# Kernel tuning notes

Measured on AMD Instinct MI355X. Metric: run time of the kernel, lower is better.

The kernel has to match this reference:

```python
import jax, jax.numpy as jnp
import numpy as np

EPS = 1e-6
NUM_HEADS = 16

def _phi(x):
    # elu kernel feature map: elu(x) + 1 (ensures positivity)
    return jax.nn.elu(x) + 1.0

def setup_inputs() -> dict:
    key = jax.random.key(0)
    ks = jax.random.split(key, 5)
    B, S, D = 2, 2048, 1024
    scale = 1.0 / np.sqrt(D)  # mimic xavier-ish magnitude
    return {
        "x": jax.random.normal(ks[0], (B, S, D), dtype=jnp.float32),
        "Wq": jax.random.normal(ks[1], (D, D), dtype=jnp.float32) * scale,
        "bq": jnp.zeros((D,), dtype=jnp.float32),
        "Wk": jax.random.normal(ks[2], (D, D), dtype=jnp.float32) * scale,
        "bk": jnp.zeros((D,), dtype=jnp.float32),
        "Wv": jax.random.normal(ks[3], (D, D), dtype=jnp.float32) * scale,
        "bv": jnp.zeros((D,), dtype=jnp.float32),
        "Wo": jax.random.normal(ks[4], (D, D), dtype=jnp.float32) * scale,
        "bo": jnp.zeros((D,), dtype=jnp.float32),
    }

def reference(x, Wq, bq, Wk, bk, Wv, bv, Wo, bo):
    B, S, D = x.shape
    H = NUM_HEADS
    hd = D // H
    # projections (torch Linear: x @ W.T + b)
    q = (x @ Wq.T + bq).reshape(B, S, H, hd).transpose(0, 2, 1, 3)  # [B,H,S,d]
    k = (x @ Wk.T + bk).reshape(B, S, H, hd).transpose(0, 2, 1, 3)
    v = (x @ Wv.T + bv).reshape(B, S, H, hd).transpose(0, 2, 1, 3)
    q = _phi(q)
    k = _phi(k)
    # prefix sums of outer products k_t v_t^T and of k_t (causal linear attention)
    kv_cum = jnp.cumsum(k[..., :, None] * v[..., None, :], axis=2)  # [B,H,S,d,d]
    k_cum = jnp.cumsum(k, axis=2)                                   # [B,H,S,d]
    num = jnp.einsum('bhsd,bhsde->bhse', q, kv_cum)                 # [B,H,S,d]
    den = jnp.einsum('bhsd,bhsd->bhs', q, k_cum)                    # [B,H,S]
    out = num / (den[..., None] + EPS)
    out = out.transpose(0, 2, 1, 3).reshape(B, S, D)
    return out @ Wo.T + bo
```

## Files before the change

kernel.cpp:

```cpp
#include <hip/hip_runtime.h>

typedef unsigned short u16;
typedef __attribute__((ext_vector_type(8))) short bf16x8;
typedef __attribute__((ext_vector_type(4))) float f32x4;

#define DEVI static __device__ __forceinline__

DEVI u16 f2bf(float f) {
  union { float f; unsigned int u; } a; a.f = f;
  unsigned int u = a.u;
  u += 0x7fffu + ((u >> 16) & 1u);
  return (u16)(u >> 16);
}
DEVI float bf2f(u16 h) {
  union { unsigned int u; float f; } a; a.u = ((unsigned int)h) << 16;
  return a.f;
}

DEVI void gload_lds16(const u16* g, u16* l) {
  __builtin_amdgcn_global_load_lds(
      (const __attribute__((address_space(1))) void*)g,
      (__attribute__((address_space(3))) void*)l, 16, 0, 0);
}

DEVI int ldsIdx(int row, int col) {
  return ((col >> 5) << 11) + (row << 5) + (col & 31);
}

struct alignas(8) US4 { u16 a, b, c, d; };

__global__ __launch_bounds__(256) void k_cvt_all(
    const float* __restrict__ x, const float* __restrict__ Wq,
    const float* __restrict__ Wk, const float* __restrict__ Wv,
    const float* __restrict__ Wo, u16* __restrict__ xb, u16* __restrict__ Wqb,
    u16* __restrict__ Wkb, u16* __restrict__ Wvb, u16* __restrict__ Wob) {
  int i = blockIdx.x * 256 + threadIdx.x;
  const float* s;
  u16* d;
  int off;
  if (i < 1048576) {
    s = x; d = xb; off = i;
  } else {
    int j = i - 1048576;
    int w = j >> 18;
    off = j & 262143;
    s = (w == 0) ? Wq : (w == 1) ? Wk : (w == 2) ? Wv : Wo;
    d = (w == 0) ? Wqb : (w == 1) ? Wkb : (w == 2) ? Wvb : Wob;
  }
  f32x4 v = ((const f32x4*)s)[off];
  US4 o{f2bf(v[0]), f2bf(v[1]), f2bf(v[2]), f2bf(v[3])};
  ((US4*)d)[off] = o;
}

__global__ __launch_bounds__(256) void k_gemm_qkv(
    const u16* __restrict__ A, const u16* __restrict__ W,
    const float* __restrict__ bq, const float* __restrict__ bk,
    const float* __restrict__ bv, u16* __restrict__ qb, u16* __restrict__ kb,
    u16* __restrict__ ktb, u16* __restrict__ vtb) {
  __shared__ __align__(16) u16 As[128 * 32];
  __shared__ __align__(16) u16 Bs[128 * 32];
  const int tid = threadIdx.x;
  const int lane = tid & 63;
  const int wave = tid >> 6;
  const int wm = wave >> 1, wn = wave & 1;
  const int m0 = blockIdx.x * 128, n0 = blockIdx.y * 128;
  const int K = 1024;
  const int m = lane & 15, quad = lane >> 4;

  f32x4 acc[4][4];
#pragma unroll
  for (int i = 0; i < 4; i++)
#pragma unroll
    for (int j = 0; j < 4; j++) acc[i][j] = (f32x4){0.f, 0.f, 0.f, 0.f};

  const int r0 = tid >> 2;
  const int r1 = (tid + 256) >> 2;
  const int c0 = (((tid & 3) ^ (r0 & 3))) * 8;
  const u16* Ab0 = A + (size_t)(m0 + r0) * K + c0;
  const u16* Ab1 = A + (size_t)(m0 + r1) * K + c0;
  const u16* Bb0 = W + (size_t)(n0 + r0) * K + c0;
  const u16* Bb1 = W + (size_t)(n0 + r1) * K + c0;
  u16* lA0 = &As[tid * 8];
  u16* lA1 = &As[(tid + 256) * 8];
  u16* lB0 = &Bs[tid * 8];
  u16* lB1 = &Bs[(tid + 256) * 8];

  const int koff = (quad ^ (m & 3)) * 8;
  for (int k0 = 0; k0 < K; k0 += 32) {
    __syncthreads();
    gload_lds16(Ab0 + k0, lA0);
    gload_lds16(Ab1 + k0, lA1);
    gload_lds16(Bb0 + k0, lB0);
    gload_lds16(Bb1 + k0, lB1);
    __syncthreads();
    bf16x8 af[4], bfr[4];
#pragma unroll
    for (int t = 0; t < 4; t++) {
      af[t] = *(const bf16x8*)&As[(wm * 64 + t * 16 + m) * 32 + koff];
      bfr[t] = *(const bf16x8*)&Bs[(wn * 64 + t * 16 + m) * 32 + koff];
    }
#pragma unroll
    for (int i = 0; i < 4; i++)
#pragma unroll
      for (int j = 0; j < 4; j++)
        acc[i][j] = __builtin_amdgcn_mfma_f32_16x16x32_bf16(af[i], bfr[j],
                                                            acc[i][j], 0, 0, 0);
  }

  const int lr = quad * 4, lc = m;
  const int region = (int)(blockIdx.y >> 3);
  const float* bias = region == 0 ? bq : (region == 1 ? bk : bv);
#pragma unroll
  for (int j = 0; j < 4; j++) {
    const int colg = n0 + wn * 64 + j * 16 + lc;
    const int cl = colg - (region << 10);
    const float bvv = bias[cl];
#pragma unroll
    for (int i = 0; i < 4; i++) {
      const int row0 = m0 + wm * 64 + i * 16 + lr;
      float v4[4];
#pragma unroll
      for (int r = 0; r < 4; r++) {
        float v = acc[i][j][r] + bvv;
        if (region < 2) v = (v > 0.f) ? (v + 1.f) : __expf(v);
        v4[r] = v;
      }
      if (region == 0) {
#pragma unroll
        for (int r = 0; r < 4; r++)
          qb[(size_t)(row0 + r) * 1024 + cl] = f2bf(v4[r]);
      } else if (region == 1) {
#pragma unroll
        for (int r = 0; r < 4; r++)
          kb[(size_t)(row0 + r) * 1024 + cl] = f2bf(v4[r]);
        US4 o{f2bf(v4[0]), f2bf(v4[1]), f2bf(v4[2]), f2bf(v4[3])};
        *(US4*)&ktb[(size_t)cl * 4096 + row0] = o;
      } else {
        US4 o{f2bf(v4[0]), f2bf(v4[1]), f2bf(v4[2]), f2bf(v4[3])};
        *(US4*)&vtb[(size_t)cl * 4096 + row0] = o;
      }
    }
  }
}

__global__ __launch_bounds__(256) void k_gemm_out(const u16* __restrict__ A,
                                                  const u16* __restrict__ B,
                                                  const float* __restrict__ bias,
                                                  float* __restrict__ C) {
  __shared__ __align__(16) u16 As[64 * 32];
  __shared__ __align__(16) u16 Bs[128 * 32];
  const int tid = threadIdx.x;
  const int lane = tid & 63;
  const int wave = tid >> 6;
  const int wm = wave >> 1, wn = wave & 1;
  const int m0 = blockIdx.x * 64, n0 = blockIdx.y * 128;
  const int K = 1024, N = 1024;
  const int m = lane & 15, quad = lane >> 4;

  f32x4 acc[2][4];
#pragma unroll
  for (int i = 0; i < 2; i++)
#pragma unroll
    for (int j = 0; j < 4; j++) acc[i][j] = (f32x4){0.f, 0.f, 0.f, 0.f};

  const int ra = tid >> 2;
  const int rb1 = (tid + 256) >> 2;
  const int c0 = (((tid & 3) ^ (ra & 3))) * 8;
  const u16* Ap = A + (size_t)(m0 + ra) * K + c0;
  const u16* Bp0 = B + (size_t)(n0 + ra) * K + c0;
  const u16* Bp1 = B + (size_t)(n0 + rb1) * K + c0;
  u16* lA = &As[tid * 8];
  u16* lB0 = &Bs[tid * 8];
  u16* lB1 = &Bs[(tid + 256) * 8];

  const int koff = (quad ^ (m & 3)) * 8;
  for (int k0 = 0; k0 < K; k0 += 32) {
    __syncthreads();
    gload_lds16(Ap + k0, lA);
    gload_lds16(Bp0 + k0, lB0);
    gload_lds16(Bp1 + k0, lB1);
    __syncthreads();
    bf16x8 af[2], bfr[4];
#pragma unroll
    for (int i = 0; i < 2; i++)
      af[i] = *(const bf16x8*)&As[(wm * 32 + i * 16 + m) * 32 + koff];
#pragma unroll
    for (int j = 0; j < 4; j++)
      bfr[j] = *(const bf16x8*)&Bs[(wn * 64 + j * 16 + m) * 32 + koff];
#pragma unroll
    for (int i = 0; i < 2; i++)
#pragma unroll
      for (int j = 0; j < 4; j++)
        acc[i][j] = __builtin_amdgcn_mfma_f32_16x16x32_bf16(af[i], bfr[j],
                                                            acc[i][j], 0, 0, 0);
  }

#pragma unroll
  for (int j = 0; j < 4; j++) {
    const int col = n0 + wn * 64 + j * 16 + m;
    const float bv = bias[col];
#pragma unroll
    for (int i = 0; i < 2; i++) {
      const int row = m0 + wm * 32 + i * 16 + quad * 4;
#pragma unroll
      for (int r = 0; r < 4; r++)
        C[(size_t)(row + r) * N + col] = acc[i][j][r] + bv;
    }
  }
}

__global__ __launch_bounds__(256) void k_chunk2(const u16* __restrict__ ktb,
                                                const u16* __restrict__ vtb,
                                                u16* __restrict__ KVtb,
                                                float* __restrict__ Ks) {
  __shared__ __align__(16) u16 Kt[4096];
  __shared__ __align__(16) u16 Vt[4096];
  __shared__ __align__(16) u16 Ct[64 * 72];
  __shared__ float ksp[64][4];
  const int tid = threadIdx.x, lane = tid & 63, wave = tid >> 6;
  const int ci = blockIdx.x, h = blockIdx.y, b = blockIdx.z;
  const int t0 = b * 2048 + ci * 64, dB = h * 64;
  const int c = (b * 16 + h) * 32 + ci;
  const int row = tid >> 2, colr = (tid & 3) * 8;
#pragma unroll
  for (int r = 0; r < 2; r++) {
    const int col = r * 32 + colr;
    gload_lds16(ktb + (size_t)(dB + row) * 4096 + t0 + col, Kt + r * 2048 + tid * 8);
    gload_lds16(vtb + (size_t)(dB + row) * 4096 + t0 + col, Vt + r * 2048 + tid * 8);
  }
  __syncthreads();
  {
    const int rr = tid >> 2, part = tid & 3;
    float s = 0.f;
#pragma unroll
    for (int t = 0; t < 16; t++) s += bf2f(Kt[ldsIdx(rr, part * 16 + t)]);
    ksp[rr][part] = s;
  }
  __syncthreads();
  if (tid < 64)
    Ks[c * 64 + tid] = ksp[tid][0] + ksp[tid][1] + ksp[tid][2] + ksp[tid][3];

  const int wm = wave >> 1, wn = wave & 1;
  const int md0 = wm * 32, ne0 = wn * 32;
  const int m = lane & 15, quad = lane >> 4;
  f32x4 acc[2][2];
#pragma unroll
  for (int i = 0; i < 2; i++)
#pragma unroll
    for (int j = 0; j < 2; j++) acc[i][j] = (f32x4){0.f, 0.f, 0.f, 0.f};
#pragma unroll
  for (int ks = 0; ks < 2; ks++) {
    const int koff = ks * 32 + quad * 8;
    bf16x8 af[2], bfr[2];
#pragma unroll
    for (int i = 0; i < 2; i++)
      af[i] = *(const bf16x8*)&Kt[ldsIdx(md0 + i * 16 + m, koff)];
#pragma unroll
    for (int j = 0; j < 2; j++)
      bfr[j] = *(const bf16x8*)&Vt[ldsIdx(ne0 + j * 16 + m, koff)];
#pragma unroll
    for (int i = 0; i < 2; i++)
#pragma unroll
      for (int j = 0; j < 2; j++)
        acc[i][j] = __builtin_amdgcn_mfma_f32_16x16x32_bf16(af[i], bfr[j],
                                                            acc[i][j], 0, 0, 0);
  }
#pragma unroll
  for (int i = 0; i < 2; i++)
#pragma unroll
    for (int j = 0; j < 2; j++) {
      const int e = ne0 + j * 16 + m;
      const int d0 = md0 + i * 16 + quad * 4;
      US4 o{f2bf(acc[i][j][0]), f2bf(acc[i][j][1]), f2bf(acc[i][j][2]),
            f2bf(acc[i][j][3])};
      *(US4*)&Ct[e * 72 + d0] = o;
    }
  __syncthreads();
  u16* outp = KVtb + (size_t)c * 4096;
#pragma unroll
  for (int rd = 0; rd < 2; rd++) {
    const int g0 = (tid + rd * 256) * 8;
    const int e = g0 >> 6, d = g0 & 63;
    bf16x8 v = *(const bf16x8*)&Ct[e * 72 + d];
    *(bf16x8*)&outp[g0] = v;
  }
}

__global__ __launch_bounds__(256) void k_prefix(u16* __restrict__ KVtb,
                                                float* __restrict__ Ks) {
  const int slice = blockIdx.x;
  const int bh = blockIdx.y;
  const int tid = threadIdx.x;
  u16* base = KVtb + (size_t)bh * 32 * 4096 + slice * 512 + tid * 2;
  unsigned int vals[32];
#pragma unroll
  for (int ci = 0; ci < 32; ci++)
    vals[ci] = *(const unsigned int*)(base + ci * 4096);
  float r0 = 0.f, r1 = 0.f;
#pragma unroll
  for (int ci = 0; ci < 32; ci++) {
    const float v0 = bf2f((u16)(vals[ci] & 0xffffu));
    const float v1 = bf2f((u16)(vals[ci] >> 16));
    const unsigned int o = (unsigned int)f2bf(r0) | ((unsigned int)f2bf(r1) << 16);
    *(unsigned int*)(base + ci * 4096) = o;
    r0 += v0;
    r1 += v1;
  }
  if (slice == 0 && tid < 64) {
    float* p = Ks + (size_t)bh * 32 * 64 + tid;
    float zb[32];
#pragma unroll
    for (int ci = 0; ci < 32; ci++) zb[ci] = p[ci * 64];
    float zr = 0.f;
#pragma unroll
    for (int ci = 0; ci < 32; ci++) {
      p[ci * 64] = zr;
      zr += zb[ci];
    }
  }
}

__global__ __launch_bounds__(256) void k_attn2(const u16* __restrict__ qb,
                                               const u16* __restrict__ kb,
                                               const u16* __restrict__ vtb,
                                               const u16* __restrict__ KVtb,
                                               const float* __restrict__ Ksg,
                                               u16* __restrict__ Og) {
  __shared__ __align__(16) u16 Qs[4096];
  __shared__ __align__(16) u16 Kr[4096];
  __shared__ __align__(16) u16 Vt[4096];
  __shared__ __align__(16) u16 St[4096];
  __shared__ __align__(16) u16 Am[64 * 72];
  __shared__ float denp[64][4];
  __shared__ float den[64];
  __shared__ float zc[64];
  const int tid = threadIdx.x, lane = tid & 63, wave = tid >> 6;
  const int ci = blockIdx.x, h = blockIdx.y, b = blockIdx.z;
  const int t0 = b * 2048 + ci * 64, colb = h * 64;
  const int c = (b * 16 + h) * 32 + ci;
  const int row = tid >> 2, colr = (tid & 3) * 8;
#pragma unroll
  for (int r = 0; r < 2; r++) {
    const int col = r * 32 + colr;
    gload_lds16(qb + (size_t)(t0 + row) * 1024 + colb + col, Qs + r * 2048 + tid * 8);
    gload_lds16(kb + (size_t)(t0 + row) * 1024 + colb + col, Kr + r * 2048 + tid * 8);
    gload_lds16(vtb + (size_t)(colb + row) * 4096 + t0 + col, Vt + r * 2048 + tid * 8);
    gload_lds16(KVtb + (size_t)c * 4096 + row * 64 + col, St + r * 2048 + tid * 8);
  }
  if (tid < 16) *(f32x4*)&zc[tid * 4] = *(const f32x4*)&Ksg[c * 64 + tid * 4];
  __syncthreads();

  const int wm = wave >> 1, wn = wave & 1;
  const int tm0 = wm * 32, sn0 = wn * 32;
  const int m = lane & 15, quad = lane >> 4;

  f32x4 accA[2][2];
#pragma unroll
  for (int i = 0; i < 2; i++)
#pragma unroll
    for (int j = 0; j < 2; j++) accA[i][j] = (f32x4){0.f, 0.f, 0.f, 0.f};
#pragma unroll
  for (int ks = 0; ks < 2; ks++) {
    const int koff = ks * 32 + quad * 8;
    bf16x8 af[2], bfr[2];
#pragma unroll
    for (int i = 0; i < 2; i++)
      af[i] = *(const bf16x8*)&Qs[ldsIdx(tm0 + i * 16 + m, koff)];
#pragma unroll
    for (int j = 0; j < 2; j++)
      bfr[j] = *(const bf16x8*)&Kr[ldsIdx(sn0 + j * 16 + m, koff)];
#pragma unroll
    for (int i = 0; i < 2; i++)
#pragma unroll
      for (int j = 0; j < 2; j++)
        accA[i][j] = __builtin_amdgcn_mfma_f32_16x16x32_bf16(af[i], bfr[j],
                                                             accA[i][j], 0, 0, 0);
  }
#pragma unroll
  for (int i = 0; i < 2; i++)
#pragma unroll
    for (int j = 0; j < 2; j++) {
      const int s = sn0 + j * 16 + m;
#pragma unroll
      for (int r = 0; r < 4; r++) {
        const int t = tm0 + i * 16 + quad * 4 + r;
        const float v = (s <= t) ? accA[i][j][r] : 0.f;
        Am[t * 72 + s] = f2bf(v);
      }
    }
  __syncthreads();
  {
    const int rr = tid >> 2, part = tid & 3;
    float rs = 0.f, qz = 0.f;
#pragma unroll
    for (int s = 0; s < 16; s++) rs += bf2f(Am[rr * 72 + part * 16 + s]);
#pragma unroll
    for (int d = 0; d < 16; d++)
      qz += bf2f(Qs[ldsIdx(rr, part * 16 + d)]) * zc[part * 16 + d];
    denp[rr][part] = rs + qz;
  }
  __syncthreads();
  if (tid < 64)
    den[tid] =
        denp[tid][0] + denp[tid][1] + denp[tid][2] + denp[tid][3] + 1e-6f;
  __syncthreads();

  f32x4 accO[2][2];
#pragma unroll
  for (int i = 0; i < 2; i++)
#pragma unroll
    for (int j = 0; j < 2; j++) accO[i][j] = (f32x4){0.f, 0.f, 0.f, 0.f};
#pragma unroll
  for (int ks = 0; ks < 2; ks++) {
    const int koff = ks * 32 + quad * 8;
    bf16x8 afA[2], bfV[2], afQ[2], bfS[2];
#pragma unroll
    for (int i = 0; i < 2; i++) {
      afA[i] = *(const bf16x8*)&Am[(tm0 + i * 16 + m) * 72 + koff];
      afQ[i] = *(const bf16x8*)&Qs[ldsIdx(tm0 + i * 16 + m, koff)];
    }
#pragma unroll
    for (int j = 0; j < 2; j++) {
      bfV[j] = *(const bf16x8*)&Vt[ldsIdx(sn0 + j * 16 + m, koff)];
      bfS[j] = *(const bf16x8*)&St[ldsIdx(sn0 + j * 16 + m, koff)];
    }
#pragma unroll
    for (int i = 0; i < 2; i++)
#pragma unroll
      for (int j = 0; j < 2; j++) {
        accO[i][j] = __builtin_amdgcn_mfma_f32_16x16x32_bf16(afA[i], bfV[j],
                                                             accO[i][j], 0, 0, 0);
        accO[i][j] = __builtin_amdgcn_mfma_f32_16x16x32_bf16(afQ[i], bfS[j],
                                                             accO[i][j], 0, 0, 0);
      }
  }
#pragma unroll
  for (int i = 0; i < 2; i++)
#pragma unroll
    for (int r = 0; r < 4; r++) {
      const int t = tm0 + i * 16 + quad * 4 + r;
      const float inv = 1.f / den[t];
#pragma unroll
      for (int j = 0; j < 2; j++) {
        const int e = sn0 + j * 16 + m;
        Og[(size_t)(t0 + t) * 1024 + colb + e] = f2bf(accO[i][j][r] * inv);
      }
    }
}

extern "C" void kernel_launch(void* const* d_in, const int* in_sizes, int n_in,
                              void* d_out, int out_size, void* d_ws,
                              size_t ws_size, hipStream_t stream) {
  const float* x = (const float*)d_in[0];
  const float* Wq = (const float*)d_in[1];
  const float* bq = (const float*)d_in[2];
  const float* Wk = (const float*)d_in[3];
  const float* bk = (const float*)d_in[4];
  const float* Wv = (const float*)d_in[5];
  const float* bv = (const float*)d_in[6];
  const float* Wo = (const float*)d_in[7];
  const float* bo = (const float*)d_in[8];

  char* ws = (char*)d_ws;
  u16* xb = (u16*)(ws + 0);
  u16* ab = xb;
  u16* Wqb = (u16*)(ws + 8388608);
  u16* Wkb = (u16*)(ws + 10485760);
  u16* Wvb = (u16*)(ws + 12582912);
  u16* Wob = (u16*)(ws + 14680064);
  u16* qb = (u16*)(ws + 16777216);
  u16* kb = (u16*)(ws + 25165824);
  u16* ktb = (u16*)(ws + 33554432);
  u16* vtb = (u16*)(ws + 41943040);
  u16* KVtb = (u16*)(ws + 50331648);
  float* Ks = (float*)(ws + 58720256);

  k_cvt_all<<<8192, 256, 0, stream>>>(x, Wq, Wk, Wv, Wo, xb, Wqb, Wkb, Wvb,
                                      Wob);

  k_gemm_qkv<<<dim3(32, 24), 256, 0, stream>>>(xb, Wqb, bq, bk, bv, qb, kb,
                                               ktb, vtb);

  dim3 ga(32, 16, 2);
  k_chunk2<<<ga, 256, 0, stream>>>(ktb, vtb, KVtb, Ks);
  k_prefix<<<dim3(8, 32), 256, 0, stream>>>(KVtb, Ks);
  k_attn2<<<ga, 256, 0, stream>>>(qb, kb, vtb, KVtb, Ks, ab);

  k_gemm_out<<<dim3(64, 8), 256, 0, stream>>>(ab, Wob, bo, (float*)d_out);
}
```

Measured before the change: 167.0 us.

## Fuse chunk prefix scan into k_chunk2 via last-block atomic ticket

Removes the separate k_prefix launch. Each k_chunk2 block takes an atomic ticket per (batch, head), and the last block to finish does the prefix scan over all 32 chunk KV states and the K sums. This saves a kernel launch and the gap between kernels, but the scan now runs in only 32 blocks instead of 256, which serialises more work per block. It also adds a memset for the counters.

```diff
diff --git a/kernel.cpp b/kernel.cpp
--- a/kernel.cpp
+++ b/kernel.cpp
@@ -212,11 +212,13 @@
 __global__ __launch_bounds__(256) void k_chunk2(const u16* __restrict__ ktb,
                                                 const u16* __restrict__ vtb,
                                                 u16* __restrict__ KVtb,
-                                                float* __restrict__ Ks) {
+                                                float* __restrict__ Ks,
+                                                unsigned int* __restrict__ cnt) {
   __shared__ __align__(16) u16 Kt[4096];
   __shared__ __align__(16) u16 Vt[4096];
   __shared__ __align__(16) u16 Ct[64 * 72];
   __shared__ float ksp[64][4];
+  __shared__ unsigned int ticket;
   const int tid = threadIdx.x, lane = tid & 63, wave = tid >> 6;
   const int ci = blockIdx.x, h = blockIdx.y, b = blockIdx.z;
   const int t0 = b * 2048 + ci * 64, dB = h * 64;
@@ -284,38 +286,44 @@
     bf16x8 v = *(const bf16x8*)&Ct[e * 72 + d];
     *(bf16x8*)&outp[g0] = v;
   }
-}
-
-__global__ __launch_bounds__(256) void k_prefix(u16* __restrict__ KVtb,
-                                                float* __restrict__ Ks) {
-  const int slice = blockIdx.x;
-  const int bh = blockIdx.y;
-  const int tid = threadIdx.x;
-  u16* base = KVtb + (size_t)bh * 32 * 4096 + slice * 512 + tid * 2;
-  unsigned int vals[32];
-#pragma unroll
-  for (int ci = 0; ci < 32; ci++)
-    vals[ci] = *(const unsigned int*)(base + ci * 4096);
-  float r0 = 0.f, r1 = 0.f;
-#pragma unroll
-  for (int ci = 0; ci < 32; ci++) {
-    const float v0 = bf2f((u16)(vals[ci] & 0xffffu));
-    const float v1 = bf2f((u16)(vals[ci] >> 16));
-    const unsigned int o = (unsigned int)f2bf(r0) | ((unsigned int)f2bf(r1) << 16);
-    *(unsigned int*)(base + ci * 4096) = o;
-    r0 += v0;
-    r1 += v1;
-  }
-  if (slice == 0 && tid < 64) {
-    float* p = Ks + (size_t)bh * 32 * 64 + tid;
-    float zb[32];
-#pragma unroll
-    for (int ci = 0; ci < 32; ci++) zb[ci] = p[ci * 64];
-    float zr = 0.f;
-#pragma unroll
-    for (int ci = 0; ci < 32; ci++) {
-      p[ci * 64] = zr;
-      zr += zb[ci];
+
+  const int bh = b * 16 + h;
+  __threadfence();
+  __syncthreads();
+  if (tid == 0) ticket = atomicAdd(&cnt[bh], 1u);
+  __syncthreads();
+  if (ticket != 31u) return;
+  __threadfence();
+  {
+    unsigned int* base = (unsigned int*)(KVtb + (size_t)bh * 32 * 4096);
+#pragma unroll
+    for (int cc = 0; cc < 8; cc++) {
+      unsigned int* p = base + tid + cc * 256;
+      unsigned int vals[32];
+#pragma unroll
+      for (int cj = 0; cj < 32; cj++) vals[cj] = p[cj * 2048];
+      float r0 = 0.f, r1 = 0.f;
+#pragma unroll
+      for (int cj = 0; cj < 32; cj++) {
+        const float v0 = bf2f((u16)(vals[cj] & 0xffffu));
+        const float v1 = bf2f((u16)(vals[cj] >> 16));
+        p[cj * 2048] =
+            (unsigned int)f2bf(r0) | ((unsigned int)f2bf(r1) << 16);
+        r0 += v0;
+        r1 += v1;
+      }
+    }
+    if (tid < 64) {
+      float* p = Ks + (size_t)bh * 32 * 64 + tid;
+      float zb[32];
+#pragma unroll
+      for (int cj = 0; cj < 32; cj++) zb[cj] = p[cj * 64];
+      float zr = 0.f;
+#pragma unroll
+      for (int cj = 0; cj < 32; cj++) {
+        p[cj * 64] = zr;
+        zr += zb[cj];
+      }
     }
   }
 }
@@ -474,6 +482,9 @@
   u16* vtb = (u16*)(ws + 41943040);
   u16* KVtb = (u16*)(ws + 50331648);
   float* Ks = (float*)(ws + 58720256);
+  unsigned int* cnt = (unsigned int*)(ws + 58982400);
+
+  hipMemsetAsync(cnt, 0, 128, stream);
 
   k_cvt_all<<<8192, 256, 0, stream>>>(x, Wq, Wk, Wv, Wo, xb, Wqb, Wkb, Wvb,
                                       Wob);
@@ -482,8 +493,7 @@
                                                ktb, vtb);
 
   dim3 ga(32, 16, 2);
-  k_chunk2<<<ga, 256, 0, stream>>>(ktb, vtb, KVtb, Ks);
-  k_prefix<<<dim3(8, 32), 256, 0, stream>>>(KVtb, Ks);
+  k_chunk2<<<ga, 256, 0, stream>>>(ktb, vtb, KVtb, Ks, cnt);
   k_attn2<<<ga, 256, 0, stream>>>(qb, kb, vtb, KVtb, Ks, ab);
 
   k_gemm_out<<<dim3(64, 8), 256, 0, stream>>>(ab, Wob, bo, (float*)d_out);
```

After: 296.9 us. +77.8%, slower.
